# Kernel optimization log

Measured on AMD Instinct MI355X. Metric: run time of the kernel, lower is better.

## Reference

```python
import jax, jax.numpy as jnp
import numpy as np

B, T, N, C, H, E, HEADS, HOR = 4, 12, 2000, 8, 64, 32000, 8, 12


def setup_inputs():
    ks = iter(jax.random.split(jax.random.key(0), 64))

    def rn(shape, s=0.05):
        return jax.random.normal(next(ks), shape, dtype=jnp.float32) * s

    inp = {}
    inp["x"] = jax.random.normal(next(ks), (B, T, N, C), dtype=jnp.float32)
    inp["edge_index"] = jax.random.randint(next(ks), (2, E), 0, N, dtype=jnp.int32)
    inp["up_w"], inp["up_b"] = rn((C, H)), rn((H,))
    for p in ("sp1", "sp2"):
        inp[p + "_msg_w1"], inp[p + "_msg_b1"] = rn((2 * H, H // 2)), rn((H // 2,))
        inp[p + "_msg_w2"], inp[p + "_msg_b2"] = rn((H // 2, H)), rn((H,))
        inp[p + "_gate_w"], inp[p + "_gate_b"] = rn((H, 1)), rn((1,))
        inp[p + "_upd_w1"], inp[p + "_upd_b1"] = rn((2 * H, H)), rn((H,))
        inp[p + "_upd_w2"], inp[p + "_upd_b2"] = rn((H, H)), rn((H,))
    for p in ("tp_wq", "tp_wk", "tp_wv", "tp_wo"):
        inp[p] = rn((H, H))
    for p in ("tp_bq", "tp_bk", "tp_bv", "tp_bo"):
        inp[p] = rn((H,))
    inp["conv_w"], inp["conv_b"] = rn((HOR, T)), rn((HOR,))
    inp["mlp_w1"], inp["mlp_b1"] = rn((H + C, H)), rn((H,))
    inp["mlp_w2"], inp["mlp_b2"] = rn((H, C)), rn((C,))
    return inp


def _spatial(h, src, tgt, mw1, mb1, mw2, mb2, gw, gb, uw1, ub1, uw2, ub2):
    # gather along node axis (node_dim=-2): x_i = target feats, x_j = source feats, [B,T,E,H]
    xi = h[:, :, tgt, :]
    xj = h[:, :, src, :]
    m = jax.nn.silu(jnp.concatenate([xi, xj], -1) @ mw1 + mb1)
    m = jax.nn.silu(m @ mw2 + mb2)
    msg = jax.nn.sigmoid(m @ gw + gb) * m            # gated message
    agg = jnp.zeros_like(h).at[:, :, tgt, :].add(msg)  # scatter-add to target nodes
    u = jax.nn.silu(jnp.concatenate([agg, h], -1) @ uw1 + ub1) @ uw2 + ub2
    return u + h  # identity skip (input_size == output_size)


def _temporal(h, wq, bq, wk, bk, wv, bv, wo, bo):
    # multi-head self-attention over the time axis, independently per node
    b, t, n, d = h.shape
    hd = d // HEADS
    q = (h @ wq + bq).reshape(b, t, n, HEADS, hd)
    k = (h @ wk + bk).reshape(b, t, n, HEADS, hd)
    v = (h @ wv + bv).reshape(b, t, n, HEADS, hd)
    scores = jnp.einsum('bsnhd,btnhd->bnhst', q, k) / jnp.sqrt(jnp.float32(hd))
    a = jax.nn.softmax(scores, axis=-1)
    o = jnp.einsum('bnhst,btnhd->bsnhd', a, v).reshape(b, t, n, d)
    return o @ wo + bo


def _forward(x, up_w, up_b,
             sp1_msg_w1, sp1_msg_b1, sp1_msg_w2, sp1_msg_b2, sp1_gate_w, sp1_gate_b,
             sp1_upd_w1, sp1_upd_b1, sp1_upd_w2, sp1_upd_b2,
             sp2_msg_w1, sp2_msg_b1, sp2_msg_w2, sp2_msg_b2, sp2_gate_w, sp2_gate_b,
             sp2_upd_w1, sp2_upd_b1, sp2_upd_w2, sp2_upd_b2,
             tp_wq, tp_bq, tp_wk, tp_bk, tp_wv, tp_bv, tp_wo, tp_bo,
             conv_w, conv_b, mlp_w1, mlp_b1, mlp_w2, mlp_b2, src, tgt):
    h = jax.nn.relu(x @ up_w + up_b)
    h = _spatial(h, src, tgt, sp1_msg_w1, sp1_msg_b1, sp1_msg_w2, sp1_msg_b2,
                 sp1_gate_w, sp1_gate_b, sp1_upd_w1, sp1_upd_b1, sp1_upd_w2, sp1_upd_b2)
    h = jax.nn.relu(h)
    h = _temporal(h, tp_wq, tp_bq, tp_wk, tp_bk, tp_wv, tp_bv, tp_wo, tp_bo)
    h = _spatial(h, src, tgt, sp2_msg_w1, sp2_msg_b1, sp2_msg_w2, sp2_msg_b2,
                 sp2_gate_w, sp2_gate_b, sp2_upd_w1, sp2_upd_b1, sp2_upd_w2, sp2_upd_b2)
    h = jax.nn.relu(h)
    z = jnp.concatenate([h, x], -1)                   # [B,T,N,H+C]
    # Conv2d(window, horizon, 1): 1x1 conv mixing the time-channel axis
    out = jnp.einsum('btnc,ht->bhnc', z, conv_w) + conv_b[None, :, None, None]
    out = jax.nn.relu(out @ mlp_w1 + mlp_b1) @ mlp_w2 + mlp_b2
    return out  # [B,HOR,N,C]


def reference(x, edge_index, up_w, up_b,
              sp1_msg_w1, sp1_msg_b1, sp1_msg_w2, sp1_msg_b2, sp1_gate_w, sp1_gate_b,
              sp1_upd_w1, sp1_upd_b1, sp1_upd_w2, sp1_upd_b2,
              sp2_msg_w1, sp2_msg_b1, sp2_msg_w2, sp2_msg_b2, sp2_gate_w, sp2_gate_b,
              sp2_upd_w1, sp2_upd_b1, sp2_upd_w2, sp2_upd_b2,
              tp_wq, tp_bq, tp_wk, tp_bk, tp_wv, tp_bv, tp_wo, tp_bo,
              conv_w, conv_b, mlp_w1, mlp_b1, mlp_w2, mlp_b2):
    src, tgt = edge_index[0], edge_index[1]
    return _forward(x, up_w, up_b,
                    sp1_msg_w1, sp1_msg_b1, sp1_msg_w2, sp1_msg_b2, sp1_gate_w, sp1_gate_b,
                    sp1_upd_w1, sp1_upd_b1, sp1_upd_w2, sp1_upd_b2,
                    sp2_msg_w1, sp2_msg_b1, sp2_msg_w2, sp2_msg_b2, sp2_gate_w, sp2_gate_b,
                    sp2_upd_w1, sp2_upd_b1, sp2_upd_w2, sp2_upd_b2,
                    tp_wq, tp_bq, tp_wk, tp_bk, tp_wv, tp_bv, tp_wo, tp_bo,
                    conv_w, conv_b, mlp_w1, mlp_b1, mlp_w2, mlp_b2, src, tgt)
```

## Files before the change

### kernel.cpp

```cpp
#include <hip/hip_runtime.h>
#include <math.h>

#define BB 4
#define TT 12
#define NN 2000
#define CC 8
#define HH 64
#define EE 32000
#define NHEADS 8
#define HD 8
#define HORZ 12
#define BT (BB*TT)
#define RR (BT*NN)

using bf16x8 = __attribute__((ext_vector_type(8))) __bf16;
using f16x8  = __attribute__((ext_vector_type(8))) _Float16;
using f16x4  = __attribute__((ext_vector_type(4))) _Float16;
using f32x4  = __attribute__((ext_vector_type(4))) float;

__device__ __forceinline__ float sigmoidf_(float x){ return 1.0f/(1.0f+__expf(-x)); }
__device__ __forceinline__ float siluf_(float x){ return x/(1.0f+__expf(-x)); }

__global__ void k_hist(const int* __restrict__ eidx, int* __restrict__ cnt) {
    int e = blockIdx.x*blockDim.x + threadIdx.x;
    if (e < EE) atomicAdd(&cnt[eidx[EE + e]], 1);
}

__global__ __launch_bounds__(256) void k_scan(const int* __restrict__ cnt,
                                              int* __restrict__ ofs_work) {
    __shared__ int part[256];
    int tid = threadIdx.x;
    int local[8]; int s = 0;
    #pragma unroll
    for (int k = 0; k < 8; ++k) {
        int idx = tid*8 + k;
        int v = (idx < NN) ? cnt[idx] : 0;
        local[k] = s; s += v;
    }
    part[tid] = s; __syncthreads();
    for (int off = 1; off < 256; off <<= 1) {
        int v = part[tid];
        int u = (tid >= off) ? part[tid-off] : 0;
        __syncthreads();
        part[tid] = v + u;
        __syncthreads();
    }
    int excl = part[tid] - s;
    #pragma unroll
    for (int k = 0; k < 8; ++k) {
        int idx = tid*8 + k;
        if (idx < NN) ofs_work[idx] = excl + local[k];
    }
}

__global__ void k_scatter(const int* __restrict__ eidx, int* __restrict__ ofs_work,
                          int* __restrict__ ssrc, int* __restrict__ stgt) {
    int e = blockIdx.x*blockDim.x + threadIdx.x;
    if (e >= EE) return;
    int t = eidx[EE + e];
    int pos = atomicAdd(&ofs_work[t], 1);
    ssrc[pos] = eidx[e];
    stgt[pos] = t;
}

__global__ void k_wprep(
    const float* __restrict__ mw2_0, const float* __restrict__ mw2_1,
    const float* __restrict__ uw1_0, const float* __restrict__ uw1_1,
    const float* __restrict__ uw2_0, const float* __restrict__ uw2_1,
    const float* __restrict__ wq, const float* __restrict__ wk,
    const float* __restrict__ wv, const float* __restrict__ wo,
    const float* __restrict__ mw1_0, const float* __restrict__ mw1_1,
    __bf16* __restrict__ mw2t0, __bf16* __restrict__ mw2t1,
    _Float16* __restrict__ uw1t0, _Float16* __restrict__ uw1t1,
    _Float16* __restrict__ uw2t0, _Float16* __restrict__ uw2t1,
    _Float16* __restrict__ qkvt, _Float16* __restrict__ wot,
    _Float16* __restrict__ mw1t0, _Float16* __restrict__ mw1t1)
{
    int i = blockIdx.x*blockDim.x + threadIdx.x;
    if (i < 2048) {
        int n = i >> 5, k = i & 31;
        mw2t0[i] = (__bf16)mw2_0[k*64 + n];
        mw2t1[i] = (__bf16)mw2_1[k*64 + n];
        return;
    }
    i -= 2048;
    if (i < 8192) {
        int n = i >> 7, k = i & 127;
        uw1t0[i] = (_Float16)uw1_0[k*64 + n];
        uw1t1[i] = (_Float16)uw1_1[k*64 + n];
        return;
    }
    i -= 8192;
    if (i < 4096) {
        int n = i >> 6, k = i & 63;
        uw2t0[i] = (_Float16)uw2_0[k*64 + n];
        uw2t1[i] = (_Float16)uw2_1[k*64 + n];
        wot[i]   = (_Float16)wo[k*64 + n];
        qkvt[i]        = (_Float16)wq[k*64 + n];
        qkvt[4096 + i] = (_Float16)wk[k*64 + n];
        qkvt[8192 + i] = (_Float16)wv[k*64 + n];
        mw1t0[i] = (_Float16)((n < 32) ? mw1_0[k*32 + n] : mw1_0[(64 + k)*32 + n - 32]);
        mw1t1[i] = (_Float16)((n < 32) ? mw1_1[k*32 + n] : mw1_1[(64 + k)*32 + n - 32]);
    }
}

__global__ void k_up(const float* __restrict__ x, const float* __restrict__ w,
                     const float* __restrict__ b, float* __restrict__ h) {
    int gid = blockIdx.x*blockDim.x + threadIdx.x;
    int wv_ = gid >> 6; int j = gid & 63;
    int r0 = wv_*4;
    if (r0 >= RR) return;
    r0 = __builtin_amdgcn_readfirstlane(r0);
    const float* xr = x + (size_t)r0*CC;
    float bj = b[j];
    float a0=bj,a1=bj,a2=bj,a3=bj;
    #pragma unroll
    for (int c = 0; c < CC; ++c) {
        float wc = w[c*HH + j];
        a0 += xr[c]*wc; a1 += xr[CC+c]*wc; a2 += xr[2*CC+c]*wc; a3 += xr[3*CC+c]*wc;
    }
    h[(size_t)r0*HH + j]        = fmaxf(a0, 0.f);
    h[(size_t)r0*HH + HH + j]   = fmaxf(a1, 0.f);
    h[(size_t)r0*HH + 2*HH + j] = fmaxf(a2, 0.f);
    h[(size_t)r0*HH + 3*HH + j] = fmaxf(a3, 0.f);
}

__device__ __forceinline__ f16x8 load_a_f16(const float* __restrict__ p) {
    f32x4 lo = *(const f32x4*)p, hi = *(const f32x4*)(p + 4);
    f16x8 v;
    #pragma unroll
    for (int u = 0; u < 4; ++u) { v[u] = (_Float16)lo[u]; v[4+u] = (_Float16)hi[u]; }
    return v;
}

__global__ __launch_bounds__(64) void k_prem(
    const float* __restrict__ h, const _Float16* __restrict__ mw1t,
    _Float16* __restrict__ preB)
{
    int t = threadIdx.x; int l15 = t & 15, quad = t >> 4;
    size_t R0 = (size_t)blockIdx.x*32;
    f32x4 acc[2][4];
    #pragma unroll
    for (int mi = 0; mi < 2; ++mi)
        #pragma unroll
        for (int ni = 0; ni < 4; ++ni) acc[mi][ni] = (f32x4){0.f,0.f,0.f,0.f};
    #pragma unroll
    for (int kc = 0; kc < 2; ++kc) {
        f16x8 a[2];
        #pragma unroll
        for (int mi = 0; mi < 2; ++mi)
            a[mi] = load_a_f16(h + (R0 + 16*mi + l15)*HH + kc*32 + quad*8);
        #pragma unroll
        for (int ni = 0; ni < 4; ++ni) {
            f16x8 b = *(const f16x8*)&mw1t[(16*ni + l15)*64 + kc*32 + quad*8];
            #pragma unroll
            for (int mi = 0; mi < 2; ++mi)
                acc[mi][ni] = __builtin_amdgcn_mfma_f32_16x16x32_f16(a[mi], b, acc[mi][ni], 0,0,0);
        }
    }
    #pragma unroll
    for (int mi = 0; mi < 2; ++mi)
        #pragma unroll
        for (int ni = 0; ni < 4; ++ni) {
            int col = 16*ni + l15;
            #pragma unroll
            for (int rg = 0; rg < 4; ++rg) {
                int row = 16*mi + 4*quad + rg;
                preB[(R0 + row)*HH + col] = (_Float16)acc[mi][ni][rg];
            }
        }
}

__global__ __launch_bounds__(64) void k_qkvm(
    const float* __restrict__ h, const _Float16* __restrict__ qkvt,
    const float* __restrict__ bq, const float* __restrict__ bk,
    const float* __restrict__ bv,
    float* __restrict__ q, float* __restrict__ k, float* __restrict__ v)
{
    int t = threadIdx.x; int l15 = t & 15, quad = t >> 4;
    size_t R0 = (size_t)blockIdx.x*32;
    f16x8 a[2][2];
    #pragma unroll
    for (int kc = 0; kc < 2; ++kc)
        #pragma unroll
        for (int mi = 0; mi < 2; ++mi)
            a[kc][mi] = load_a_f16(h + (R0 + 16*mi + l15)*HH + kc*32 + quad*8);

    const float* bias[3] = {bq, bk, bv};
    float* outp[3] = {q, k, v};
    #pragma unroll
    for (int o = 0; o < 3; ++o) {
        f32x4 acc[2][4];
        #pragma unroll
        for (int mi = 0; mi < 2; ++mi)
            #pragma unroll
            for (int ni = 0; ni < 4; ++ni) acc[mi][ni] = (f32x4){0.f,0.f,0.f,0.f};
        #pragma unroll
        for (int kc = 0; kc < 2; ++kc)
            #pragma unroll
            for (int ni = 0; ni < 4; ++ni) {
                f16x8 b = *(const f16x8*)&qkvt[o*4096 + (16*ni + l15)*64 + kc*32 + quad*8];
                #pragma unroll
                for (int mi = 0; mi < 2; ++mi)
                    acc[mi][ni] = __builtin_amdgcn_mfma_f32_16x16x32_f16(a[kc][mi], b, acc[mi][ni], 0,0,0);
            }
        #pragma unroll
        for (int mi = 0; mi < 2; ++mi)
            #pragma unroll
            for (int ni = 0; ni < 4; ++ni) {
                int col = 16*ni + l15;
                float bb = bias[o][col];
                #pragma unroll
                for (int rg = 0; rg < 4; ++rg) {
                    int row = 16*mi + 4*quad + rg;
                    outp[o][(R0 + row)*HH + col] = acc[mi][ni][rg] + bb;
                }
            }
    }
}

__global__ __launch_bounds__(64) void k_updm(
    const float* __restrict__ agg, const float* __restrict__ h,
    const _Float16* __restrict__ w1t, const float* __restrict__ b1,
    const _Float16* __restrict__ w2t, const float* __restrict__ b2,
    float* __restrict__ out, int do_relu)
{
    __shared__ _Float16 uS[32][72];
    int t = threadIdx.x; int l15 = t & 15, quad = t >> 4;
    size_t R0 = (size_t)blockIdx.x*32;

    f32x4 acc[2][4];
    #pragma unroll
    for (int mi = 0; mi < 2; ++mi)
        #pragma unroll
        for (int ni = 0; ni < 4; ++ni) acc[mi][ni] = (f32x4){0.f,0.f,0.f,0.f};
    #pragma unroll
    for (int kc = 0; kc < 4; ++kc) {
        const float* src = (kc < 2) ? agg : h;
        int colb = (kc & 1)*32 + quad*8;
        f16x8 a[2];
        #pragma unroll
        for (int mi = 0; mi < 2; ++mi)
            a[mi] = load_a_f16(src + (R0 + 16*mi + l15)*HH + colb);
        #pragma unroll
        for (int ni = 0; ni < 4; ++ni) {
            f16x8 b = *(const f16x8*)&w1t[(16*ni + l15)*128 + kc*32 + quad*8];
            #pragma unroll
            for (int mi = 0; mi < 2; ++mi)
                acc[mi][ni] = __builtin_amdgcn_mfma_f32_16x16x32_f16(a[mi], b, acc[mi][ni], 0,0,0);
        }
    }
    #pragma unroll
    for (int mi = 0; mi < 2; ++mi)
        #pragma unroll
        for (int ni = 0; ni < 4; ++ni) {
            int col = 16*ni + l15;
            float bb = b1[col];
            #pragma unroll
            for (int rg = 0; rg < 4; ++rg)
                uS[16*mi + 4*quad + rg][col] = (_Float16)siluf_(acc[mi][ni][rg] + bb);
        }
    __syncthreads();

    f32x4 acc2[2][4];
    #pragma unroll
    for (int mi = 0; mi < 2; ++mi)
        #pragma unroll
        for (int ni = 0; ni < 4; ++ni) acc2[mi][ni] = (f32x4){0.f,0.f,0.f,0.f};
    #pragma unroll
    for (int kc = 0; kc < 2; ++kc) {
        f16x8 a[2];
        #pragma unroll
        for (int mi = 0; mi < 2; ++mi)
            a[mi] = *(const f16x8*)&uS[16*mi + l15][kc*32 + quad*8];
        #pragma unroll
        for (int ni = 0; ni < 4; ++ni) {
            f16x8 b = *(const f16x8*)&w2t[(16*ni + l15)*64 + kc*32 + quad*8];
            #pragma unroll
            for (int mi = 0; mi < 2; ++mi)
                acc2[mi][ni] = __builtin_amdgcn_mfma_f32_16x16x32_f16(a[mi], b, acc2[mi][ni], 0,0,0);
        }
    }
    #pragma unroll
    for (int mi = 0; mi < 2; ++mi)
        #pragma unroll
        for (int ni = 0; ni < 4; ++ni) {
            int col = 16*ni + l15;
            float bb = b2[col];
            #pragma unroll
            for (int rg = 0; rg < 4; ++rg) {
                int row = 16*mi + 4*quad + rg;
                float o = acc2[mi][ni][rg] + bb + h[(R0 + row)*HH + col];
                if (do_relu) o = fmaxf(o, 0.f);
                out[(R0 + row)*HH + col] = o;
            }
        }
}

__global__ __launch_bounds__(64) void k_wopre(
    const float* __restrict__ ob, const _Float16* __restrict__ wot,
    const float* __restrict__ bo, const _Float16* __restrict__ mw1t,
    float* __restrict__ aout, _Float16* __restrict__ preB)
{
    __shared__ _Float16 hS[32][72];
    int t = threadIdx.x; int l15 = t & 15, quad = t >> 4;
    size_t R0 = (size_t)blockIdx.x*32;

    f32x4 acc[2][4];
    #pragma unroll
    for (int mi = 0; mi < 2; ++mi)
        #pragma unroll
        for (int ni = 0; ni < 4; ++ni) acc[mi][ni] = (f32x4){0.f,0.f,0.f,0.f};
    #pragma unroll
    for (int kc = 0; kc < 2; ++kc) {
        f16x8 a[2];
        #pragma unroll
        for (int mi = 0; mi < 2; ++mi)
            a[mi] = load_a_f16(ob + (R0 + 16*mi + l15)*HH + kc*32 + quad*8);
        #pragma unroll
        for (int ni = 0; ni < 4; ++ni) {
            f16x8 b = *(const f16x8*)&wot[(16*ni + l15)*64 + kc*32 + quad*8];
            #pragma unroll
            for (int mi = 0; mi < 2; ++mi)
                acc[mi][ni] = __builtin_amdgcn_mfma_f32_16x16x32_f16(a[mi], b, acc[mi][ni], 0,0,0);
        }
    }
    #pragma unroll
    for (int mi = 0; mi < 2; ++mi)
        #pragma unroll
        for (int ni = 0; ni < 4; ++ni) {
            int col = 16*ni + l15;
            float bb = bo[col];
            #pragma unroll
            for (int rg = 0; rg < 4; ++rg) {
                int row = 16*mi + 4*quad + rg;
                float o = acc[mi][ni][rg] + bb;
                aout[(R0 + row)*HH + col] = o;
                hS[row][col] = (_Float16)o;
            }
        }
    __syncthreads();

    f32x4 acc2[2][4];
    #pragma unroll
    for (int mi = 0; mi < 2; ++mi)
        #pragma unroll
        for (int ni = 0; ni < 4; ++ni) acc2[mi][ni] = (f32x4){0.f,0.f,0.f,0.f};
    #pragma unroll
    for (int kc = 0; kc < 2; ++kc) {
        f16x8 a[2];
        #pragma unroll
        for (int mi = 0; mi < 2; ++mi)
            a[mi] = *(const f16x8*)&hS[16*mi + l15][kc*32 + quad*8];
        #pragma unroll
        for (int ni = 0; ni < 4; ++ni) {
            f16x8 b = *(const f16x8*)&mw1t[(16*ni + l15)*64 + kc*32 + quad*8];
            #pragma unroll
            for (int mi = 0; mi < 2; ++mi)
                acc2[mi][ni] = __builtin_amdgcn_mfma_f32_16x16x32_f16(a[mi], b, acc2[mi][ni], 0,0,0);
        }
    }
    #pragma unroll
    for (int mi = 0; mi < 2; ++mi)
        #pragma unroll
        for (int ni = 0; ni < 4; ++ni) {
            int col = 16*ni + l15;
            #pragma unroll
            for (int rg = 0; rg < 4; ++rg) {
                int row = 16*mi + 4*quad + rg;
                preB[(R0 + row)*HH + col] = (_Float16)acc2[mi][ni][rg];
            }
        }
}

__global__ __launch_bounds__(64) void k_msg(
    const _Float16* __restrict__ preB, const int* __restrict__ ssrc,
    const int* __restrict__ stgt,
    const float* __restrict__ b1,
    const __bf16* __restrict__ w2t, const float* __restrict__ b2,
    const float* __restrict__ gw, const float* __restrict__ gb,
    float* __restrict__ agg)
{
    int bt = blockIdx.x % BT;
    int eb = blockIdx.x / BT;
    int t  = threadIdx.x;
    int l15 = t & 15, quad = t >> 4;

    union __align__(16) SM {
        __bf16   ab[64][40];
        _Float16 bs[8][64][8];
    };
    __shared__ SM sm;
    __shared__ int segTgt[64];

    int e0 = eb*64;
    int my_src = ssrc[e0 + t];
    int my_tgt = stgt[e0 + t];

    int prevt = __shfl(my_tgt, (t + 63) & 63);
    bool bnd = (t == 0) || (prevt != my_tgt);
    unsigned long long bm = __ballot(bnd);
    int seg = __builtin_amdgcn_mbcnt_hi((unsigned)(bm >> 32),
              __builtin_amdgcn_mbcnt_lo((unsigned)bm, 0u));
    int nseg = __popcll(bm);
    if (bnd) segTgt[seg] = my_tgt;

    const _Float16* basep = preB + (size_t)bt*NN*HH;
    const _Float16* rT = basep + (size_t)my_tgt*HH;
    const _Float16* rS = basep + (size_t)my_src*HH + 32;
    f16x8 xi[4], xj[4];
    #pragma unroll
    for (int g4 = 0; g4 < 4; ++g4) {
        xi[g4] = *(const f16x8*)&rT[8*g4];
        xj[g4] = *(const f16x8*)&rS[8*g4];
    }
    #pragma unroll
    for (int g4 = 0; g4 < 4; ++g4) {
        bf16x8 v;
        #pragma unroll
        for (int u = 0; u < 8; ++u) {
            float m = (float)xi[g4][u] + (float)xj[g4][u] + b1[8*g4 + u];
            v[u] = (__bf16)siluf_(m);
        }
        ((bf16x8*)&sm.ab[t][0])[g4] = v;
    }

    bf16x8 bfr[4];
    float b2v[4], gwv[4];
    #pragma unroll
    for (int ni = 0; ni < 4; ++ni) {
        bfr[ni] = *(const bf16x8*)&w2t[(16*ni + l15)*32 + quad*8];
        b2v[ni] = b2[16*ni + l15];
        gwv[ni] = gw[16*ni + l15];
    }
    float gb0 = gb[0];

    __syncthreads();

    f32x4 acc[4][4];
    #pragma unroll
    for (int mi = 0; mi < 4; ++mi) {
        bf16x8 af = *(const bf16x8*)&sm.ab[16*mi + l15][quad*8];
        #pragma unroll
        for (int ni = 0; ni < 4; ++ni) {
            f32x4 z = {0.f, 0.f, 0.f, 0.f};
            acc[mi][ni] = __builtin_amdgcn_mfma_f32_16x16x32_bf16(af, bfr[ni], z, 0, 0, 0);
        }
    }
    __syncthreads();

    #pragma unroll
    for (int mi = 0; mi < 4; ++mi) {
        float sv[4][4];
        #pragma unroll
        for (int ni = 0; ni < 4; ++ni)
            #pragma unroll
            for (int rg = 0; rg < 4; ++rg)
                sv[ni][rg] = siluf_(acc[mi][ni][rg] + b2v[ni]);
        float gg[4];
        #pragma unroll
        for (int rg = 0; rg < 4; ++rg) {
            float p = sv[0][rg]*gwv[0] + sv[1][rg]*gwv[1]
                    + sv[2][rg]*gwv[2] + sv[3][rg]*gwv[3];
            p += __shfl_xor(p, 1); p += __shfl_xor(p, 2);
            p += __shfl_xor(p, 4); p += __shfl_xor(p, 8);
            gg[rg] = sigmoidf_(p + gb0);
        }
        int c  = mi >> 1;
        int qb = 2*(mi & 1) + (quad >> 1);
        int j0 = 4*(quad & 1);
        #pragma unroll
        for (int ni = 0; ni < 4; ++ni) {
            f16x4 pk;
            #pragma unroll
            for (int rg = 0; rg < 4; ++rg) pk[rg] = (_Float16)(sv[ni][rg]*gg[rg]);
            *(f16x4*)&sm.bs[c*4 + ni][16*qb + l15][j0] = pk;
        }
    }
    __syncthreads();

    f16x8 bfrag[2][4];
    #pragma unroll
    for (int c = 0; c < 2; ++c)
        #pragma unroll
        for (int ni = 0; ni < 4; ++ni)
            bfrag[c][ni] = *(const f16x8*)&sm.bs[c*4 + ni][t][0];

    float* ap = agg + (size_t)bt*NN*HH;
    for (int g0 = 0; g0 < nseg; g0 += 16) {
        f16x8 ind[2];
        #pragma unroll
        for (int c = 0; c < 2; ++c) {
            #pragma unroll
            for (int j = 0; j < 8; ++j) {
                int sj = __shfl(seg, 32*c + 8*quad + j);
                ind[c][j] = (sj == g0 + l15) ? (_Float16)1.0f : (_Float16)0.0f;
            }
        }
        f32x4 av[4];
        #pragma unroll
        for (int ni = 0; ni < 4; ++ni) {
            f32x4 z = {0.f, 0.f, 0.f, 0.f};
            av[ni] = __builtin_amdgcn_mfma_f32_16x16x32_f16(ind[0], bfrag[0][ni], z, 0, 0, 0);
            av[ni] = __builtin_amdgcn_mfma_f32_16x16x32_f16(ind[1], bfrag[1][ni], av[ni], 0, 0, 0);
        }
        #pragma unroll
        for (int rg = 0; rg < 4; ++rg) {
            int s = g0 + 4*quad + rg;
            if (s < nseg) {
                int tn = segTgt[s];
                #pragma unroll
                for (int ni = 0; ni < 4; ++ni)
                    atomicAdd(&ap[(size_t)tn*HH + 16*ni + l15], av[ni][rg]);
            }
        }
    }
}

__global__ __launch_bounds__(64) void k_attn2(
    const float* __restrict__ q, const float* __restrict__ k,
    const float* __restrict__ v, float* __restrict__ o)
{
    __shared__ float Qs[TT][68], Ks[TT][68], Vs[TT][68], Os[TT][68];
    int p = blockIdx.x;
    int b = p / NN, n = p % NN;
    int j = threadIdx.x;
    const size_t stride = (size_t)NN*HH;
    const size_t base0  = ((size_t)(b*TT)*NN + n)*HH;

    #pragma unroll
    for (int t = 0; t < TT; ++t) {
        size_t off = base0 + (size_t)t*stride + j;
        Qs[t][j] = q[off];
        Ks[t][j] = k[off];
        Vs[t][j] = v[off];
    }
    __syncthreads();

    #pragma unroll
    for (int half = 0; half < 2; ++half) {
        if (j < 48) {
            int head = half*4 + j/12;
            int s    = j % 12;
            f32x4 qv0 = *(const f32x4*)&Qs[s][head*8];
            f32x4 qv1 = *(const f32x4*)&Qs[s][head*8 + 4];
            float sc[TT]; float mx = -1e30f;
            #pragma unroll
            for (int t = 0; t < TT; ++t) {
                f32x4 k0 = *(const f32x4*)&Ks[t][head*8];
                f32x4 k1 = *(const f32x4*)&Ks[t][head*8 + 4];
                float a = qv0[0]*k0[0] + qv0[1]*k0[1] + qv0[2]*k0[2] + qv0[3]*k0[3]
                        + qv1[0]*k1[0] + qv1[1]*k1[1] + qv1[2]*k1[2] + qv1[3]*k1[3];
                a *= 0.35355339059327373f;
                sc[t] = a; mx = fmaxf(mx, a);
            }
            float sum = 0.f;
            #pragma unroll
            for (int t = 0; t < TT; ++t) { sc[t] = __expf(sc[t]-mx); sum += sc[t]; }
            float inv = 1.0f/sum;
            f32x4 o0 = {0.f,0.f,0.f,0.f}, o1 = {0.f,0.f,0.f,0.f};
            #pragma unroll
            for (int t = 0; t < TT; ++t) {
                float a = sc[t]*inv;
                f32x4 v0 = *(const f32x4*)&Vs[t][head*8];
                f32x4 v1 = *(const f32x4*)&Vs[t][head*8 + 4];
                o0[0]+=a*v0[0]; o0[1]+=a*v0[1]; o0[2]+=a*v0[2]; o0[3]+=a*v0[3];
                o1[0]+=a*v1[0]; o1[1]+=a*v1[1]; o1[2]+=a*v1[2]; o1[3]+=a*v1[3];
            }
            *(f32x4*)&Os[s][head*8]     = o0;
            *(f32x4*)&Os[s][head*8 + 4] = o1;
        }
    }
    __syncthreads();

    #pragma unroll
    for (int t = 0; t < TT; ++t)
        o[base0 + (size_t)t*stride + j] = Os[t][j];
}

__global__ __launch_bounds__(256) void k_zbuild(
    const float* __restrict__ h, const float* __restrict__ x,
    const float* __restrict__ cw, const float* __restrict__ cb,
    float* __restrict__ z)
{
    int gid = blockIdx.x*blockDim.x + threadIdx.x;
    int p = gid >> 6;
    int j = gid & 63;
    if (p >= BB*NN) return;
    p = __builtin_amdgcn_readfirstlane(p);
    int b = p / NN, n = p % NN;

    float hv[TT];
    #pragma unroll
    for (int t = 0; t < TT; ++t)
        hv[t] = h[((size_t)(b*TT + t)*NN + n)*HH + j];
    float xv[TT];
    if (j < CC) {
        #pragma unroll
        for (int t = 0; t < TT; ++t)
            xv[t] = x[((size_t)(b*TT + t)*NN + n)*CC + j];
    }

    #pragma unroll
    for (int hor = 0; hor < HORZ; ++hor) {
        float cbv = cb[hor];
        float zh = cbv, zx = cbv;
        #pragma unroll
        for (int t = 0; t < TT; ++t) {
            float w = cw[hor*TT + t];
            zh += w*hv[t];
            if (j < CC) zx += w*xv[t];
        }
        size_t row = (size_t)(b*HORZ + hor)*NN + n;
        z[row*72 + j] = zh;
        if (j < CC) z[row*72 + 64 + j] = zx;
    }
}

__global__ __launch_bounds__(256) void k_headmlp(
    const float* __restrict__ z,
    const float* __restrict__ w1, const float* __restrict__ b1,
    const float* __restrict__ w2, const float* __restrict__ b2,
    float* __restrict__ out)
{
    __shared__ float U[4][4][65];
    int gid = blockIdx.x*blockDim.x + threadIdx.x;
    int wv_ = gid >> 6; int j = gid & 63;
    int wl = threadIdx.x >> 6;
    int r0 = wv_*4;
    r0 = __builtin_amdgcn_readfirstlane(r0);
    const float* zr = z + (size_t)r0*72;
    float bj = b1[j];
    float a0=bj,a1=bj,a2=bj,a3=bj;
    #pragma unroll 8
    for (int c = 0; c < 72; ++c) {
        float wc = w1[c*64 + j];
        a0 += zr[c]*wc; a1 += zr[72+c]*wc; a2 += zr[144+c]*wc; a3 += zr[216+c]*wc;
    }
    U[wl][0][j] = fmaxf(a0, 0.f);
    U[wl][1][j] = fmaxf(a1, 0.f);
    U[wl][2][j] = fmaxf(a2, 0.f);
    U[wl][3][j] = fmaxf(a3, 0.f);
    __syncthreads();

    if (j < 32) {
        int r = j >> 3, c = j & 7;
        float o = b2[c];
        #pragma unroll 8
        for (int k = 0; k < 64; ++k)
            o += U[wl][r][k] * w2[k*8 + c];
        out[(size_t)(r0 + r)*CC + c] = o;
    }
}

extern "C" void kernel_launch(void* const* d_in, const int* in_sizes, int n_in,
                              void* d_out, int out_size, void* d_ws, size_t ws_size,
                              hipStream_t stream) {
    const float* x    = (const float*)d_in[0];
    const int*   eidx = (const int*)d_in[1];
    const float* up_w = (const float*)d_in[2];
    const float* up_b = (const float*)d_in[3];
    const float* sp_w[2][10];
    for (int p = 0; p < 2; ++p)
        for (int i = 0; i < 10; ++i)
            sp_w[p][i] = (const float*)d_in[4 + p*10 + i];
    const float* wq = (const float*)d_in[24];
    const float* wk = (const float*)d_in[25];
    const float* wv = (const float*)d_in[26];
    const float* wo = (const float*)d_in[27];
    const float* bq = (const float*)d_in[28];
    const float* bk = (const float*)d_in[29];
    const float* bv = (const float*)d_in[30];
    const float* bo = (const float*)d_in[31];
    const float* conv_w = (const float*)d_in[32];
    const float* conv_b = (const float*)d_in[33];
    const float* mlp_w1 = (const float*)d_in[34];
    const float* mlp_b1 = (const float*)d_in[35];
    const float* mlp_w2 = (const float*)d_in[36];
    const float* mlp_b2 = (const float*)d_in[37];
    float* out = (float*)d_out;

    const size_t BUF = (size_t)RR*HH;
    float* A    = (float*)d_ws;
    float* Bb   = A   + BUF;
    float* AGG  = Bb  + BUF;
    float* Vb   = AGG + BUF;
    float* Ob   = Vb  + BUF;
    _Float16* PRE = (_Float16*)(Ob + BUF);
    int*   cnt      = (int*)(PRE + BUF);
    int*   ofs_work = cnt + 2048;
    int*   ssrc     = ofs_work + 2048;
    int*   stgt     = ssrc + EE;
    __bf16* mw2t0   = (__bf16*)(stgt + EE);
    __bf16* mw2t1   = mw2t0 + 2048;
    _Float16* uw1t0 = (_Float16*)(mw2t1 + 2048);
    _Float16* uw1t1 = uw1t0 + 8192;
    _Float16* uw2t0 = uw1t1 + 8192;
    _Float16* uw2t1 = uw2t0 + 4096;
    _Float16* qkvt  = uw2t1 + 4096;
    _Float16* wot   = qkvt + 3*4096;
    _Float16* mw1t0 = wot + 4096;
    _Float16* mw1t1 = mw1t0 + 4096;
    float* Z = AGG;

    const int G4 = RR/16;
    const int GT = RR/32;

    hipMemsetAsync(cnt, 0, 2048*sizeof(int), stream);
    k_hist<<<(EE+255)/256, 256, 0, stream>>>(eidx, cnt);
    k_wprep<<<56, 256, 0, stream>>>(
        sp_w[0][2], sp_w[1][2], sp_w[0][6], sp_w[1][6], sp_w[0][8], sp_w[1][8],
        wq, wk, wv, wo, sp_w[0][0], sp_w[1][0],
        mw2t0, mw2t1, uw1t0, uw1t1, uw2t0, uw2t1, qkvt, wot, mw1t0, mw1t1);
    k_scan<<<1, 256, 0, stream>>>(cnt, ofs_work);
    k_scatter<<<(EE+255)/256, 256, 0, stream>>>(eidx, ofs_work, ssrc, stgt);

    k_up<<<G4, 256, 0, stream>>>(x, up_w, up_b, A);
    k_prem<<<GT, 64, 0, stream>>>(A, mw1t0, PRE);

    hipMemsetAsync(AGG, 0, BUF*sizeof(float), stream);
    k_msg<<<BT*(EE/64), 64, 0, stream>>>(PRE, ssrc, stgt,
        sp_w[0][1], mw2t0, sp_w[0][3], sp_w[0][4], sp_w[0][5], AGG);
    k_updm<<<GT, 64, 0, stream>>>(AGG, A, uw1t0, sp_w[0][7], uw2t0, sp_w[0][9], Bb, 1);

    k_qkvm<<<GT, 64, 0, stream>>>(Bb, qkvt, bq, bk, bv, A, AGG, Vb);
    k_attn2<<<BB*NN, 64, 0, stream>>>(A, AGG, Vb, Ob);
    k_wopre<<<GT, 64, 0, stream>>>(Ob, wot, bo, mw1t1, A, PRE);

    hipMemsetAsync(AGG, 0, BUF*sizeof(float), stream);
    k_msg<<<BT*(EE/64), 64, 0, stream>>>(PRE, ssrc, stgt,
        sp_w[1][1], mw2t1, sp_w[1][3], sp_w[1][4], sp_w[1][5], AGG);
    k_updm<<<GT, 64, 0, stream>>>(AGG, A, uw1t1, sp_w[1][7], uw2t1, sp_w[1][9], Bb, 1);

    k_zbuild<<<(BB*NN*64 + 255)/256, 256, 0, stream>>>(Bb, x, conv_w, conv_b, Z);
    k_headmlp<<<(BB*HORZ*NN)/16, 256, 0, stream>>>(Z,
        mlp_w1, mlp_b1, mlp_w2, mlp_b2, out);
}
```

Measured before the change: 505.4 us.

## Fuse up-projection with message pre-GEMM, and spatial update with QKV projection

The scalar up-projection kernel is replaced by an MFMA GEMM over a zero-padded K=32 fp16 weight, prepared in the weight-prep kernel. It is fused with the first message pre-GEMM, which now reads h from LDS in fp16 instead of re-reading it from global memory. The first spatial update kernel is fused with the Q/K/V projection, so the updated hidden state stays in LDS and is never written to or re-read from global memory. Outputs alias the inputs (q into A, k into AGG), which relies on each block touching only its own rows, with reads completing before the barrier.

```diff
diff --git a/kernel.cpp b/kernel.cpp
--- a/kernel.cpp
+++ b/kernel.cpp
@@ -70,11 +70,13 @@
     const float* __restrict__ wq, const float* __restrict__ wk,
     const float* __restrict__ wv, const float* __restrict__ wo,
     const float* __restrict__ mw1_0, const float* __restrict__ mw1_1,
+    const float* __restrict__ up_w,
     __bf16* __restrict__ mw2t0, __bf16* __restrict__ mw2t1,
     _Float16* __restrict__ uw1t0, _Float16* __restrict__ uw1t1,
     _Float16* __restrict__ uw2t0, _Float16* __restrict__ uw2t1,
     _Float16* __restrict__ qkvt, _Float16* __restrict__ wot,
-    _Float16* __restrict__ mw1t0, _Float16* __restrict__ mw1t1)
+    _Float16* __restrict__ mw1t0, _Float16* __restrict__ mw1t1,
+    _Float16* __restrict__ upwt)
 {
     int i = blockIdx.x*blockDim.x + threadIdx.x;
     if (i < 2048) {
@@ -101,28 +103,13 @@
         qkvt[8192 + i] = (_Float16)wv[k*64 + n];
         mw1t0[i] = (_Float16)((n < 32) ? mw1_0[k*32 + n] : mw1_0[(64 + k)*32 + n - 32]);
         mw1t1[i] = (_Float16)((n < 32) ? mw1_1[k*32 + n] : mw1_1[(64 + k)*32 + n - 32]);
-    }
-}
-
-__global__ void k_up(const float* __restrict__ x, const float* __restrict__ w,
-                     const float* __restrict__ b, float* __restrict__ h) {
-    int gid = blockIdx.x*blockDim.x + threadIdx.x;
-    int wv_ = gid >> 6; int j = gid & 63;
-    int r0 = wv_*4;
-    if (r0 >= RR) return;
-    r0 = __builtin_amdgcn_readfirstlane(r0);
-    const float* xr = x + (size_t)r0*CC;
-    float bj = b[j];
-    float a0=bj,a1=bj,a2=bj,a3=bj;
-    #pragma unroll
-    for (int c = 0; c < CC; ++c) {
-        float wc = w[c*HH + j];
-        a0 += xr[c]*wc; a1 += xr[CC+c]*wc; a2 += xr[2*CC+c]*wc; a3 += xr[3*CC+c]*wc;
-    }
-    h[(size_t)r0*HH + j]        = fmaxf(a0, 0.f);
-    h[(size_t)r0*HH + HH + j]   = fmaxf(a1, 0.f);
-    h[(size_t)r0*HH + 2*HH + j] = fmaxf(a2, 0.f);
-    h[(size_t)r0*HH + 3*HH + j] = fmaxf(a3, 0.f);
+        return;
+    }
+    i -= 4096;
+    if (i < 2048) {
+        int n = i >> 5, k = i & 31;
+        upwt[i] = (k < CC) ? (_Float16)up_w[k*64 + n] : (_Float16)0.0f;
+    }
 }
 
 __device__ __forceinline__ f16x8 load_a_f16(const float* __restrict__ p) {
@@ -133,68 +120,186 @@
     return v;
 }
 
-__global__ __launch_bounds__(64) void k_prem(
-    const float* __restrict__ h, const _Float16* __restrict__ mw1t,
-    _Float16* __restrict__ preB)
+__global__ __launch_bounds__(64) void k_upre(
+    const float* __restrict__ x, const _Float16* __restrict__ upwt,
+    const float* __restrict__ upb, const _Float16* __restrict__ mw1t,
+    float* __restrict__ h, _Float16* __restrict__ preB)
 {
+    __shared__ _Float16 hS[32][72];
     int t = threadIdx.x; int l15 = t & 15, quad = t >> 4;
     size_t R0 = (size_t)blockIdx.x*32;
+
+    f16x8 a[2];
+    #pragma unroll
+    for (int mi = 0; mi < 2; ++mi) {
+        f16x8 v;
+        #pragma unroll
+        for (int u = 0; u < 8; ++u) v[u] = (_Float16)0.0f;
+        if (quad == 0) {
+            const float* xr = x + (R0 + 16*mi + l15)*CC;
+            f32x4 lo = *(const f32x4*)xr, hi = *(const f32x4*)(xr + 4);
+            #pragma unroll
+            for (int u = 0; u < 4; ++u) { v[u] = (_Float16)lo[u]; v[4+u] = (_Float16)hi[u]; }
+        }
+        a[mi] = v;
+    }
     f32x4 acc[2][4];
     #pragma unroll
     for (int mi = 0; mi < 2; ++mi)
         #pragma unroll
         for (int ni = 0; ni < 4; ++ni) acc[mi][ni] = (f32x4){0.f,0.f,0.f,0.f};
     #pragma unroll
-    for (int kc = 0; kc < 2; ++kc) {
-        f16x8 a[2];
-        #pragma unroll
-        for (int mi = 0; mi < 2; ++mi)
-            a[mi] = load_a_f16(h + (R0 + 16*mi + l15)*HH + kc*32 + quad*8);
-        #pragma unroll
-        for (int ni = 0; ni < 4; ++ni) {
-            f16x8 b = *(const f16x8*)&mw1t[(16*ni + l15)*64 + kc*32 + quad*8];
-            #pragma unroll
-            for (int mi = 0; mi < 2; ++mi)
-                acc[mi][ni] = __builtin_amdgcn_mfma_f32_16x16x32_f16(a[mi], b, acc[mi][ni], 0,0,0);
-        }
+    for (int ni = 0; ni < 4; ++ni) {
+        f16x8 b = *(const f16x8*)&upwt[(16*ni + l15)*32 + quad*8];
+        #pragma unroll
+        for (int mi = 0; mi < 2; ++mi)
+            acc[mi][ni] = __builtin_amdgcn_mfma_f32_16x16x32_f16(a[mi], b, acc[mi][ni], 0,0,0);
     }
     #pragma unroll
     for (int mi = 0; mi < 2; ++mi)
         #pragma unroll
         for (int ni = 0; ni < 4; ++ni) {
             int col = 16*ni + l15;
+            float bb = upb[col];
             #pragma unroll
             for (int rg = 0; rg < 4; ++rg) {
                 int row = 16*mi + 4*quad + rg;
-                preB[(R0 + row)*HH + col] = (_Float16)acc[mi][ni][rg];
-            }
-        }
-}
-
-__global__ __launch_bounds__(64) void k_qkvm(
-    const float* __restrict__ h, const _Float16* __restrict__ qkvt,
+                float o = fmaxf(acc[mi][ni][rg] + bb, 0.f);
+                h[(R0 + row)*HH + col] = o;
+                hS[row][col] = (_Float16)o;
+            }
+        }
+    __syncthreads();
+
+    f32x4 acc2[2][4];
+    #pragma unroll
+    for (int mi = 0; mi < 2; ++mi)
+        #pragma unroll
+        for (int ni = 0; ni < 4; ++ni) acc2[mi][ni] = (f32x4){0.f,0.f,0.f,0.f};
+    #pragma unroll
+    for (int kc = 0; kc < 2; ++kc) {
+        f16x8 av[2];
+        #pragma unroll
+        for (int mi = 0; mi < 2; ++mi)
+            av[mi] = *(const f16x8*)&hS[16*mi + l15][kc*32 + quad*8];
+        #pragma unroll
+        for (int ni = 0; ni < 4; ++ni) {
+            f16x8 b = *(const f16x8*)&mw1t[(16*ni + l15)*64 + kc*32 + quad*8];
+            #pragma unroll
+            for (int mi = 0; mi < 2; ++mi)
+                acc2[mi][ni] = __builtin_amdgcn_mfma_f32_16x16x32_f16(av[mi], b, acc2[mi][ni], 0,0,0);
+        }
+    }
+    #pragma unroll
+    for (int mi = 0; mi < 2; ++mi)
+        #pragma unroll
+        for (int ni = 0; ni < 4; ++ni) {
+            int col = 16*ni + l15;
+            #pragma unroll
+            for (int rg = 0; rg < 4; ++rg) {
+                int row = 16*mi + 4*quad + rg;
+                preB[(R0 + row)*HH + col] = (_Float16)acc2[mi][ni][rg];
+            }
+        }
+}
+
+__global__ __launch_bounds__(64) void k_updqkv(
+    const float* __restrict__ agg, const float* __restrict__ h,
+    const _Float16* __restrict__ w1t, const float* __restrict__ b1,
+    const _Float16* __restrict__ w2t, const float* __restrict__ b2,
+    const _Float16* __restrict__ qkvt,
     const float* __restrict__ bq, const float* __restrict__ bk,
     const float* __restrict__ bv,
     float* __restrict__ q, float* __restrict__ k, float* __restrict__ v)
 {
+    __shared__ _Float16 uS[32][72];
+    __shared__ _Float16 hS[32][72];
     int t = threadIdx.x; int l15 = t & 15, quad = t >> 4;
     size_t R0 = (size_t)blockIdx.x*32;
+
+    f32x4 acc[2][4];
+    #pragma unroll
+    for (int mi = 0; mi < 2; ++mi)
+        #pragma unroll
+        for (int ni = 0; ni < 4; ++ni) acc[mi][ni] = (f32x4){0.f,0.f,0.f,0.f};
+    #pragma unroll
+    for (int kc = 0; kc < 4; ++kc) {
+        const float* src = (kc < 2) ? agg : h;
+        int colb = (kc & 1)*32 + quad*8;
+        f16x8 a[2];
+        #pragma unroll
+        for (int mi = 0; mi < 2; ++mi)
+            a[mi] = load_a_f16(src + (R0 + 16*mi + l15)*HH + colb);
+        #pragma unroll
+        for (int ni = 0; ni < 4; ++ni) {
+            f16x8 b = *(const f16x8*)&w1t[(16*ni + l15)*128 + kc*32 + quad*8];
+            #pragma unroll
+            for (int mi = 0; mi < 2; ++mi)
+                acc[mi][ni] = __builtin_amdgcn_mfma_f32_16x16x32_f16(a[mi], b, acc[mi][ni], 0,0,0);
+        }
+    }
+    #pragma unroll
+    for (int mi = 0; mi < 2; ++mi)
+        #pragma unroll
+        for (int ni = 0; ni < 4; ++ni) {
+            int col = 16*ni + l15;
+            float bb = b1[col];
+            #pragma unroll
+            for (int rg = 0; rg < 4; ++rg)
+                uS[16*mi + 4*quad + rg][col] = (_Float16)siluf_(acc[mi][ni][rg] + bb);
+        }
+    __syncthreads();
+
+    f32x4 acc2[2][4];
+    #pragma unroll
+    for (int mi = 0; mi < 2; ++mi)
+        #pragma unroll
+        for (int ni = 0; ni < 4; ++ni) acc2[mi][ni] = (f32x4){0.f,0.f,0.f,0.f};
+    #pragma unroll
+    for (int kc = 0; kc < 2; ++kc) {
+        f16x8 a[2];
+        #pragma unroll
+        for (int mi = 0; mi < 2; ++mi)
+            a[mi] = *(const f16x8*)&uS[16*mi + l15][kc*32 + quad*8];
+        #pragma unroll
+        for (int ni = 0; ni < 4; ++ni) {
+            f16x8 b = *(const f16x8*)&w2t[(16*ni + l15)*64 + kc*32 + quad*8];
+            #pragma unroll
+            for (int mi = 0; mi < 2; ++mi)
+                acc2[mi][ni] = __builtin_amdgcn_mfma_f32_16x16x32_f16(a[mi], b, acc2[mi][ni], 0,0,0);
+        }
+    }
+    #pragma unroll
+    for (int mi = 0; mi < 2; ++mi)
+        #pragma unroll
+        for (int ni = 0; ni < 4; ++ni) {
+            int col = 16*ni + l15;
+            float bb = b2[col];
+            #pragma unroll
+            for (int rg = 0; rg < 4; ++rg) {
+                int row = 16*mi + 4*quad + rg;
+                float o = acc2[mi][ni][rg] + bb + h[(R0 + row)*HH + col];
+                hS[row][col] = (_Float16)fmaxf(o, 0.f);
+            }
+        }
+    __syncthreads();
+
     f16x8 a[2][2];
     #pragma unroll
     for (int kc = 0; kc < 2; ++kc)
         #pragma unroll
         for (int mi = 0; mi < 2; ++mi)
-            a[kc][mi] = load_a_f16(h + (R0 + 16*mi + l15)*HH + kc*32 + quad*8);
+            a[kc][mi] = *(const f16x8*)&hS[16*mi + l15][kc*32 + quad*8];
 
     const float* bias[3] = {bq, bk, bv};
     float* outp[3] = {q, k, v};
     #pragma unroll
     for (int o = 0; o < 3; ++o) {
-        f32x4 acc[2][4];
-        #pragma unroll
-        for (int mi = 0; mi < 2; ++mi)
-            #pragma unroll
-            for (int ni = 0; ni < 4; ++ni) acc[mi][ni] = (f32x4){0.f,0.f,0.f,0.f};
+        f32x4 ac[2][4];
+        #pragma unroll
+        for (int mi = 0; mi < 2; ++mi)
+            #pragma unroll
+            for (int ni = 0; ni < 4; ++ni) ac[mi][ni] = (f32x4){0.f,0.f,0.f,0.f};
         #pragma unroll
         for (int kc = 0; kc < 2; ++kc)
             #pragma unroll
@@ -202,7 +307,7 @@
                 f16x8 b = *(const f16x8*)&qkvt[o*4096 + (16*ni + l15)*64 + kc*32 + quad*8];
                 #pragma unroll
                 for (int mi = 0; mi < 2; ++mi)
-                    acc[mi][ni] = __builtin_amdgcn_mfma_f32_16x16x32_f16(a[kc][mi], b, acc[mi][ni], 0,0,0);
+                    ac[mi][ni] = __builtin_amdgcn_mfma_f32_16x16x32_f16(a[kc][mi], b, ac[mi][ni], 0,0,0);
             }
         #pragma unroll
         for (int mi = 0; mi < 2; ++mi)
@@ -213,7 +318,7 @@
                 #pragma unroll
                 for (int rg = 0; rg < 4; ++rg) {
                     int row = 16*mi + 4*quad + rg;
-                    outp[o][(R0 + row)*HH + col] = acc[mi][ni][rg] + bb;
+                    outp[o][(R0 + row)*HH + col] = ac[mi][ni][rg] + bb;
                 }
             }
     }
@@ -701,29 +806,29 @@
     _Float16* wot   = qkvt + 3*4096;
     _Float16* mw1t0 = wot + 4096;
     _Float16* mw1t1 = mw1t0 + 4096;
+    _Float16* upwt  = mw1t1 + 4096;
     float* Z = AGG;
 
-    const int G4 = RR/16;
     const int GT = RR/32;
 
     hipMemsetAsync(cnt, 0, 2048*sizeof(int), stream);
     k_hist<<<(EE+255)/256, 256, 0, stream>>>(eidx, cnt);
-    k_wprep<<<56, 256, 0, stream>>>(
+    k_wprep<<<64, 256, 0, stream>>>(
         sp_w[0][2], sp_w[1][2], sp_w[0][6], sp_w[1][6], sp_w[0][8], sp_w[1][8],
-        wq, wk, wv, wo, sp_w[0][0], sp_w[1][0],
-        mw2t0, mw2t1, uw1t0, uw1t1, uw2t0, uw2t1, qkvt, wot, mw1t0, mw1t1);
+        wq, wk, wv, wo, sp_w[0][0], sp_w[1][0], up_w,
+        mw2t0, mw2t1, uw1t0, uw1t1, uw2t0, uw2t1, qkvt, wot, mw1t0, mw1t1, upwt);
     k_scan<<<1, 256, 0, stream>>>(cnt, ofs_work);
     k_scatter<<<(EE+255)/256, 256, 0, stream>>>(eidx, ofs_work, ssrc, stgt);
 
-    k_up<<<G4, 256, 0, stream>>>(x, up_w, up_b, A);
-    k_prem<<<GT, 64, 0, stream>>>(A, mw1t0, PRE);
+    k_upre<<<GT, 64, 0, stream>>>(x, upwt, up_b, mw1t0, A, PRE);
 
     hipMemsetAsync(AGG, 0, BUF*sizeof(float), stream);
     k_msg<<<BT*(EE/64), 64, 0, stream>>>(PRE, ssrc, stgt,
         sp_w[0][1], mw2t0, sp_w[0][3], sp_w[0][4], sp_w[0][5], AGG);
-    k_updm<<<GT, 64, 0, stream>>>(AGG, A, uw1t0, sp_w[0][7], uw2t0, sp_w[0][9], Bb, 1);
-
-    k_qkvm<<<GT, 64, 0, stream>>>(Bb, qkvt, bq, bk, bv, A, AGG, Vb);
+    k_updqkv<<<GT, 64, 0, stream>>>(AGG, A,
+        uw1t0, sp_w[0][7], uw2t0, sp_w[0][9],
+        qkvt, bq, bk, bv, A, AGG, Vb);
+
     k_attn2<<<BB*NN, 64, 0, stream>>>(A, AGG, Vb, Ob);
     k_wopre<<<GT, 64, 0, stream>>>(Ob, wot, bo, mw1t1, A, PRE);
 
```

After: 493.0 us, median of 2. 1.03x faster.
